# Performance work log

Measured on AMD Instinct MI355X. Metric: run time of the kernel, lower is better.

## Reference

```python
import jax, jax.numpy as jnp
import numpy as np

HEADS = 8

def setup_inputs() -> dict:
    key = jax.random.key(0)
    ks = jax.random.split(key, 5)
    B, C, H, W = 2, 256, 64, 64
    dim = C
    x = jax.random.normal(ks[0], (B, C, H, W), dtype=jnp.float32)
    # Linear weights stored as [in, out] so y = x @ W + b
    w_qkv = jax.random.normal(ks[1], (dim, 3 * dim), dtype=jnp.float32) * (dim ** -0.5)
    b_qkv = jax.random.normal(ks[2], (3 * dim,), dtype=jnp.float32) * 0.02
    w_out = jax.random.normal(ks[3], (dim, dim), dtype=jnp.float32) * (dim ** -0.5)
    b_out = jax.random.normal(ks[4], (dim,), dtype=jnp.float32) * 0.02
    return {"x": x, "w_qkv": w_qkv, "b_qkv": b_qkv, "w_out": w_out, "b_out": b_out}

def reference(x, w_qkv, b_qkv, w_out, b_out):
    B, C, H, W = x.shape
    h = HEADS
    d = C // h
    scale = d ** -0.5
    # [B, C, H, W] -> [B, N, C]
    tokens = x.reshape(B, C, H * W).transpose(0, 2, 1)
    qkv = tokens @ w_qkv + b_qkv  # [B, N, 3C]
    q, k, v = jnp.split(qkv, 3, axis=-1)
    def to_heads(t):
        Bn, N, _ = t.shape
        return t.reshape(Bn, N, h, d).transpose(0, 2, 1, 3)  # [B, h, N, d]
    q, k, v = map(to_heads, (q, k, v))
    dots = jnp.einsum('bhnd,bhmd->bhnm', q, k) * scale  # [B, h, N, N]
    attn = jax.nn.softmax(dots, axis=-1)
    out = jnp.einsum('bhnm,bhmd->bhnd', attn, v)  # [B, h, N, d]
    out = out.transpose(0, 2, 1, 3).reshape(B, H * W, C)  # [B, N, C]
    out = out @ w_out + b_out
    return out.transpose(0, 2, 1).reshape(B, C, H, W)
```

## Files before the change

### kernel.cpp

```cpp
#include <hip/hip_runtime.h>

typedef __attribute__((ext_vector_type(8))) short s16x8;
typedef __attribute__((ext_vector_type(4))) short s16x4;
typedef __attribute__((ext_vector_type(4))) float f32x4;
typedef __attribute__((ext_vector_type(2))) unsigned u32x2;

#define MFMA32(a, b, c) __builtin_amdgcn_mfma_f32_16x16x32_bf16((a), (b), (c), 0, 0, 0)

#if __has_builtin(__builtin_amdgcn_mfma_f32_16x16x16bf16_1k)
#define MFMA16K(a, b, c) __builtin_amdgcn_mfma_f32_16x16x16bf16_1k((a), (b), (c), 0, 0, 0)
#else
#define MFMA16K(a, b, c) (c)
#endif

#if __has_builtin(__builtin_amdgcn_exp2f)
#define EXP2F(x) __builtin_amdgcn_exp2f(x)
#else
#define EXP2F(x) __exp2f(x)
#endif

#if __has_builtin(__builtin_amdgcn_rcpf)
#define RCPF(x) __builtin_amdgcn_rcpf(x)
#else
#define RCPF(x) (1.0f / (x))
#endif

#define SL2E 0.25507313f

__device__ __forceinline__ unsigned pkrne(float a, float b) {
  unsigned ua = __builtin_bit_cast(unsigned, a);
  unsigned ub = __builtin_bit_cast(unsigned, b);
  ua += 0x7FFFu + ((ua >> 16) & 1u);
  ub += 0x7FFFu + ((ub >> 16) & 1u);
  return __builtin_amdgcn_perm(ub, ua, 0x07060302u);
}

__device__ __forceinline__ unsigned pktrunc(float a, float b) {
  return __builtin_amdgcn_perm(__builtin_bit_cast(unsigned, b),
                               __builtin_bit_cast(unsigned, a), 0x07060302u);
}

__device__ __forceinline__ unsigned short bfr(float f) {
  unsigned u = __builtin_bit_cast(unsigned, f);
  u += 0x7FFFu + ((u >> 16) & 1u);
  return (unsigned short)(u >> 16);
}

__device__ __forceinline__ float bflo(unsigned u) {
  return __builtin_bit_cast(float, u << 16);
}
__device__ __forceinline__ float bfhi(unsigned u) {
  return __builtin_bit_cast(float, u & 0xFFFF0000u);
}

__global__ __launch_bounds__(256) void prep_kernel(
    const float* __restrict__ x, const float* __restrict__ wqkv,
    const float* __restrict__ wout, ushort* __restrict__ xbf,
    ushort* __restrict__ wT, ushort* __restrict__ woT) {
  const int t = threadIdx.x;
  const int sub = t & 15, grp = t >> 4;
  const int id = blockIdx.x;
  const float* src;
  ushort* dst;
  int src_ld, k0, n0;
  float sc = 1.f;
  if (id < 512) {
    int mt = id & 63, kt = (id >> 6) & 3, b = id >> 8;
    src = x + (size_t)b * 256 * 4096;
    src_ld = 4096;
    dst = xbf + (size_t)b * 4096 * 256;
    k0 = kt * 64;
    n0 = mt * 64;
  } else if (id < 560) {
    int r = id - 512, nt = r % 12, kt = r / 12;
    src = wqkv;
    src_ld = 768;
    dst = wT;
    k0 = kt * 64;
    n0 = nt * 64;
    if (n0 < 256) sc = SL2E;
  } else {
    int r = id - 560, nt = r & 3, kt = r >> 2;
    src = wout;
    src_ld = 256;
    dst = woT;
    k0 = kt * 64;
    n0 = nt * 64;
  }
  const int k = k0 + grp * 4;
  const int n = n0 + sub * 4;
  unsigned d0[4], d1[4];
#pragma unroll
  for (int i = 0; i < 4; ++i) {
    float4 v = *(const float4*)(src + (size_t)(k + i) * src_ld + n);
    d0[i] = pkrne(v.x * sc, v.y * sc);
    d1[i] = pkrne(v.z * sc, v.w * sc);
  }
  u32x2 r0 = {__builtin_amdgcn_perm(d0[1], d0[0], 0x05040100u),
              __builtin_amdgcn_perm(d0[3], d0[2], 0x05040100u)};
  u32x2 r1 = {__builtin_amdgcn_perm(d0[1], d0[0], 0x07060302u),
              __builtin_amdgcn_perm(d0[3], d0[2], 0x07060302u)};
  u32x2 r2 = {__builtin_amdgcn_perm(d1[1], d1[0], 0x05040100u),
              __builtin_amdgcn_perm(d1[3], d1[2], 0x05040100u)};
  u32x2 r3 = {__builtin_amdgcn_perm(d1[1], d1[0], 0x07060302u),
              __builtin_amdgcn_perm(d1[3], d1[2], 0x07060302u)};
  *(u32x2*)(dst + (size_t)(n + 0) * 256 + k) = r0;
  *(u32x2*)(dst + (size_t)(n + 1) * 256 + k) = r1;
  *(u32x2*)(dst + (size_t)(n + 2) * 256 + k) = r2;
  *(u32x2*)(dst + (size_t)(n + 3) * 256 + k) = r3;
}

__global__ __launch_bounds__(256) void qkv_kernel(
    const ushort* __restrict__ xbf, const ushort* __restrict__ wT,
    const float* __restrict__ bq, ushort* __restrict__ QG,
    ushort* __restrict__ KG, ushort* __restrict__ VtG) {
  __shared__ __align__(16) ushort Wl[64][40];
  __shared__ __align__(16) ushort Xl[128][40];
  const int t0 = blockIdx.x * 128;
  const int n0 = blockIdx.y * 64;
  const int t = threadIdx.x;
  const int wid = t >> 6, lane = t & 63;
  const int wy = wid >> 1, wx = wid & 1;
  const int quad = lane >> 4, l16 = lane & 15;
  f32x4 acc[2][4] = {};
  const int wr = t >> 2, wsg = t & 3;
  for (int k0 = 0; k0 < 256; k0 += 32) {
    __syncthreads();
    *(uint4*)&Wl[wr][wsg * 8] =
        *(const uint4*)(wT + (size_t)(n0 + wr) * 256 + k0 + wsg * 8);
#pragma unroll
    for (int i = 0; i < 2; ++i) {
      int fid = t + 256 * i, row = fid >> 2, seg = fid & 3;
      *(uint4*)&Xl[row][seg * 8] =
          *(const uint4*)(xbf + (size_t)(t0 + row) * 256 + k0 + seg * 8);
    }
    __syncthreads();
    s16x8 wf[2], xf[4];
#pragma unroll
    for (int i = 0; i < 2; ++i)
      wf[i] = *(const s16x8*)&Wl[32 * wy + 16 * i + l16][quad * 8];
#pragma unroll
    for (int j = 0; j < 4; ++j)
      xf[j] = *(const s16x8*)&Xl[64 * wx + 16 * j + l16][quad * 8];
#pragma unroll
    for (int i = 0; i < 2; ++i)
#pragma unroll
      for (int j = 0; j < 4; ++j) acc[i][j] = MFMA32(wf[i], xf[j], acc[i][j]);
  }
  if (n0 < 512) {
    ushort* dst = (n0 < 256) ? QG : KG;
    const float bsc = (n0 < 256) ? SL2E : 1.f;
#pragma unroll
    for (int i = 0; i < 2; ++i) {
      int nb = n0 + 32 * wy + 16 * i + 4 * quad;
      float4 b4 = *(const float4*)(bq + nb);
      float bx0 = b4.x * bsc, bx1 = b4.y * bsc, bx2 = b4.z * bsc,
            bx3 = b4.w * bsc;
      int h = ((nb & 255) >> 5);
      int dd0 = nb & 31;
#pragma unroll
      for (int j = 0; j < 4; ++j) {
        int tok = t0 + 64 * wx + 16 * j + l16;
        int b = tok >> 12, tokn = tok & 4095;
        u32x2 pk = {pkrne(acc[i][j][0] + bx0, acc[i][j][1] + bx1),
                    pkrne(acc[i][j][2] + bx2, acc[i][j][3] + bx3)};
        *(u32x2*)(dst + ((size_t)(b * 8 + h) * 4096 + tokn) * 32 + dd0) = pk;
      }
    }
  } else {
#pragma unroll
    for (int i = 0; i < 2; ++i) {
      int nb = n0 + 32 * wy + 16 * i + 4 * quad;
      float4 b4 = *(const float4*)(bq + nb);
      float bb[4] = {b4.x, b4.y, b4.z, b4.w};
#pragma unroll
      for (int r = 0; r < 4; ++r) {
        int nn = nb + r - 512;
        int h = nn >> 5, ddv = nn & 31;
        ushort* vrow = VtG + (size_t)(h * 32 + ddv) * 4096;
#pragma unroll
        for (int j = 0; j < 4; ++j) {
          int tok = t0 + 64 * wx + 16 * j + l16;
          int b = tok >> 12, tokn = tok & 4095;
          vrow[(size_t)b * 8 * 32 * 4096 + tokn] = bfr(acc[i][j][r] + bb[r]);
        }
      }
    }
  }
}

__global__ __launch_bounds__(256, 6) void attn_split(
    const ushort* __restrict__ QG, const ushort* __restrict__ KG,
    const ushort* __restrict__ VtG, ushort* __restrict__ OF0,
    ushort* __restrict__ OFb, float* __restrict__ LF) {
  __shared__ __align__(16) ushort Kl[2][64][40];
  __shared__ __align__(16) ushort Vl[2][32][72];
  const int id = blockIdx.x;
  const int bh = (id & 7) * 2 + ((id >> 3) & 1);
  const int q0 = ((id >> 4) & 31) * 128;
  const int sp = id >> 9;
  const int kt0 = (sp * 64 + 2) / 3;
  const int niter = ((sp + 1) * 64 + 2) / 3 - kt0;
  const int t = threadIdx.x;
  const int wid = t >> 6, lane = t & 63;
  const int quad = lane >> 4, l16 = lane & 15;
  const size_t base = (size_t)bh * 4096 * 32;
  const ushort* qp = QG + base;
  const ushort* kp = KG + base;
  const ushort* vp = VtG + base;
  const int qw = q0 + 32 * wid;
  const s16x8 qf0 = *(const s16x8*)(qp + (size_t)(qw + l16) * 32 + quad * 8);
  const s16x8 qf1 = *(const s16x8*)(qp + (size_t)(qw + 16 + l16) * 32 + quad * 8);
  const int kr = t >> 2, ks = t & 3;
  const int vr = t >> 3, vsg = t & 7;
  *(uint4*)&Kl[0][kr][ks * 8] =
      *(const uint4*)(kp + (size_t)(kt0 * 64 + kr) * 32 + ks * 8);
  *(uint4*)&Vl[0][vr][vsg * 8] =
      *(const uint4*)(vp + (size_t)vr * 4096 + kt0 * 64 + vsg * 8);
  const ushort* kpre = kp + (size_t)((kt0 + 1) * 64 + kr) * 32 + ks * 8;
  const ushort* vpre = vp + (size_t)vr * 4096 + (kt0 + 1) * 64 + vsg * 8;
  __syncthreads();
  f32x4 o00 = {}, o01 = {}, o10 = {}, o11 = {}, ol0 = {}, ol1 = {};
  const f32x4 zero = {};
  const s16x4 ones = {(short)0x3F80, (short)0x3F80, (short)0x3F80,
                      (short)0x3F80};
  for (int i = 0; i < niter; ++i) {
    const int cur = i & 1;
    const bool more = (i + 1) < niter;
    uint4 kv, vv;
    if (more) {
      kv = *(const uint4*)kpre;
      vv = *(const uint4*)vpre;
      kpre += 2048;
      vpre += 64;
    }
    unsigned pl0[4], ph0[4], pl1[4], ph1[4];
#pragma unroll
    for (int nb = 0; nb < 4; ++nb) {
      s16x8 kf = *(const s16x8*)&Kl[cur][16 * nb + l16][quad * 8];
      f32x4 s0 = MFMA32(kf, qf0, zero);
      f32x4 s1 = MFMA32(kf, qf1, zero);
      pl0[nb] = pktrunc(EXP2F(s0[0]), EXP2F(s0[1]));
      ph0[nb] = pktrunc(EXP2F(s0[2]), EXP2F(s0[3]));
      pl1[nb] = pktrunc(EXP2F(s1[0]), EXP2F(s1[1]));
      ph1[nb] = pktrunc(EXP2F(s1[2]), EXP2F(s1[3]));
    }
#pragma unroll
    for (int nb = 0; nb < 4; ++nb) {
      u32x2 pu0 = {pl0[nb], ph0[nb]};
      u32x2 pu1 = {pl1[nb], ph1[nb]};
      s16x4 pv0 = __builtin_bit_cast(s16x4, pu0);
      s16x4 pv1 = __builtin_bit_cast(s16x4, pu1);
      s16x4 va = *(const s16x4*)&Vl[cur][l16][16 * nb + quad * 4];
      s16x4 vb = *(const s16x4*)&Vl[cur][16 + l16][16 * nb + quad * 4];
      o00 = MFMA16K(va, pv0, o00);
      o01 = MFMA16K(vb, pv0, o01);
      o10 = MFMA16K(va, pv1, o10);
      o11 = MFMA16K(vb, pv1, o11);
      ol0 = MFMA16K(ones, pv0, ol0);
      ol1 = MFMA16K(ones, pv1, ol1);
    }
    if (more) {
      *(uint4*)&Kl[cur ^ 1][kr][ks * 8] = kv;
      *(uint4*)&Vl[cur ^ 1][vr][vsg * 8] = vv;
    }
    __syncthreads();
  }
  ushort* OFs = (sp == 0) ? OF0 : OFb + (size_t)(sp - 1) * 2097152;
  float* LFs = LF + (size_t)sp * 65536;
  const int tok0 = qw + l16;
  const size_t ob0 = ((size_t)bh * 4096 + tok0) * 32;
  const size_t ob1 = ob0 + (size_t)16 * 32;
  u32x2 w00 = {pkrne(o00[0], o00[1]), pkrne(o00[2], o00[3])};
  u32x2 w01 = {pkrne(o01[0], o01[1]), pkrne(o01[2], o01[3])};
  u32x2 w10 = {pkrne(o10[0], o10[1]), pkrne(o10[2], o10[3])};
  u32x2 w11 = {pkrne(o11[0], o11[1]), pkrne(o11[2], o11[3])};
  *(u32x2*)(OFs + ob0 + 4 * quad) = w00;
  *(u32x2*)(OFs + ob0 + 16 + 4 * quad) = w01;
  *(u32x2*)(OFs + ob1 + 4 * quad) = w10;
  *(u32x2*)(OFs + ob1 + 16 + 4 * quad) = w11;
  if (quad == 0) {
    LFs[(size_t)bh * 4096 + tok0] = ol0[0];
    LFs[(size_t)bh * 4096 + tok0 + 16] = ol1[0];
  }
}

__global__ __launch_bounds__(256) void proj_split(
    const ushort* __restrict__ OF0, const ushort* __restrict__ OFb,
    const float* __restrict__ LF, const ushort* __restrict__ woT,
    const float* __restrict__ bo, float* __restrict__ out) {
  __shared__ __align__(16) ushort Wl[64][40];
  __shared__ __align__(16) ushort Xl[128][40];
  const int t0 = blockIdx.x * 128;
  const int c0 = blockIdx.y * 64;
  const int t = threadIdx.x;
  const int wid = t >> 6, lane = t & 63;
  const int wy = wid >> 1, wx = wid & 1;
  const int quad = lane >> 4, l16 = lane & 15;
  f32x4 acc[2][4] = {};
  const int wr = t >> 2, wsg = t & 3;
  const int c8 = (t & 7) * 4;
  for (int k0 = 0; k0 < 256; k0 += 32) {
    __syncthreads();
    *(uint4*)&Wl[wr][wsg * 8] =
        *(const uint4*)(woT + (size_t)(c0 + wr) * 256 + k0 + wsg * 8);
    const int hh = k0 >> 5;
#pragma unroll
    for (int p = 0; p < 4; ++p) {
      int row = 32 * p + (t >> 3);
      int tok = t0 + row, bb = tok >> 12, tokn = tok & 4095;
      size_t ro = (size_t)(bb * 8 + hh) * 4096 + tokn;
      size_t oi = ro * 32 + c8;
      uint2 a0 = *(const uint2*)(OF0 + oi);
      uint2 a1 = *(const uint2*)(OFb + oi);
      uint2 a2 = *(const uint2*)(OFb + 2097152 + oi);
      float l = LF[ro] + LF[65536 + ro] + LF[131072 + ro];
      float inv = RCPF(l);
      f32x4 s;
      s[0] = bflo(a0.x) + bflo(a1.x) + bflo(a2.x);
      s[1] = bfhi(a0.x) + bfhi(a1.x) + bfhi(a2.x);
      s[2] = bflo(a0.y) + bflo(a1.y) + bflo(a2.y);
      s[3] = bfhi(a0.y) + bfhi(a1.y) + bfhi(a2.y);
      s *= inv;
      u32x2 pk = {pkrne(s[0], s[1]), pkrne(s[2], s[3])};
      *(u32x2*)&Xl[row][c8] = pk;
    }
    __syncthreads();
    s16x8 wf[2], xf[4];
#pragma unroll
    for (int i = 0; i < 2; ++i)
      wf[i] = *(const s16x8*)&Wl[32 * wy + 16 * i + l16][quad * 8];
#pragma unroll
    for (int j = 0; j < 4; ++j)
      xf[j] = *(const s16x8*)&Xl[64 * wx + 16 * j + l16][quad * 8];
#pragma unroll
    for (int i = 0; i < 2; ++i)
#pragma unroll
      for (int j = 0; j < 4; ++j) acc[i][j] = MFMA32(wf[i], xf[j], acc[i][j]);
  }
#pragma unroll
  for (int i = 0; i < 2; ++i) {
    int cb = c0 + 32 * wy + 16 * i + 4 * quad;
    float4 b4 = *(const float4*)(bo + cb);
    float bb[4] = {b4.x, b4.y, b4.z, b4.w};
#pragma unroll
    for (int j = 0; j < 4; ++j) {
      int tok = t0 + 64 * wx + 16 * j + l16;
      int b = tok >> 12, tokn = tok & 4095;
#pragma unroll
      for (int r = 0; r < 4; ++r)
        out[((size_t)(b * 256 + cb + r)) * 4096 + tokn] = acc[i][j][r] + bb[r];
    }
  }
}

extern "C" void kernel_launch(void* const* d_in, const int* in_sizes, int n_in,
                              void* d_out, int out_size, void* d_ws, size_t ws_size,
                              hipStream_t stream) {
  (void)in_sizes; (void)n_in; (void)out_size; (void)ws_size;
  const float* x = (const float*)d_in[0];
  const float* wq = (const float*)d_in[1];
  const float* bq = (const float*)d_in[2];
  const float* wo = (const float*)d_in[3];
  const float* bo = (const float*)d_in[4];
  float* out = (float*)d_out;
  ushort* ws = (ushort*)d_ws;
  ushort* xbf = ws;
  ushort* OF0 = ws;
  ushort* QG  = ws + 2097152;
  ushort* KG  = ws + 4194304;
  ushort* VtG = ws + 6291456;
  ushort* wT  = ws + 8388608;
  ushort* woT = ws + 8585216;
  ushort* OFb = ws + 8650752;
  float* LF = (float*)(ws + 12845056);
  prep_kernel<<<576, 256, 0, stream>>>(x, wq, wo, xbf, wT, woT);
  qkv_kernel<<<dim3(64, 12), 256, 0, stream>>>(xbf, wT, bq, QG, KG, VtG);
  attn_split<<<1536, 256, 0, stream>>>(QG, KG, VtG, OF0, OFb, LF);
  proj_split<<<dim3(64, 4), 256, 0, stream>>>(OF0, OFb, LF, woT, bo, out);
}
```

Baseline: 140.0 us.

## Rework split attention around 32x32x16 MFMA with direct LDS staging

Rewrites the attention inner loop to use 32x32x16 bf16 MFMA for both the QK^T and PV products instead of 16x16 tiles. P is rearranged between the two products with permlane32 swaps rather than a round trip through memory. K/V tiles are staged straight from global memory into LDS with global_load_lds into a pre-swizzled layout. The row sum is now accumulated with VALU adds instead of an extra ones-vector MFMA. Occupancy bound drops from 6 to 4 blocks per CU, and output stores become scalar 2-byte writes, which may be less efficient.

```diff
diff --git a/kernel.cpp b/kernel.cpp
--- a/kernel.cpp
+++ b/kernel.cpp
@@ -1,16 +1,17 @@
 #include <hip/hip_runtime.h>
 
 typedef __attribute__((ext_vector_type(8))) short s16x8;
-typedef __attribute__((ext_vector_type(4))) short s16x4;
 typedef __attribute__((ext_vector_type(4))) float f32x4;
+typedef __attribute__((ext_vector_type(16))) float f32x16;
 typedef __attribute__((ext_vector_type(2))) unsigned u32x2;
+typedef __attribute__((ext_vector_type(4))) unsigned u32x4;
 
 #define MFMA32(a, b, c) __builtin_amdgcn_mfma_f32_16x16x32_bf16((a), (b), (c), 0, 0, 0)
 
-#if __has_builtin(__builtin_amdgcn_mfma_f32_16x16x16bf16_1k)
-#define MFMA16K(a, b, c) __builtin_amdgcn_mfma_f32_16x16x16bf16_1k((a), (b), (c), 0, 0, 0)
-#else
-#define MFMA16K(a, b, c) (c)
+#if __has_builtin(__builtin_amdgcn_mfma_f32_32x32x16_bf16)
+#define MFMA3216(a, b, c) __builtin_amdgcn_mfma_f32_32x32x16_bf16((a), (b), (c), 0, 0, 0)
+#else
+#define MFMA3216(a, b, c) (c)
 #endif
 
 #if __has_builtin(__builtin_amdgcn_exp2f)
@@ -51,6 +52,33 @@
 }
 __device__ __forceinline__ float bfhi(unsigned u) {
   return __builtin_bit_cast(float, u & 0xFFFF0000u);
+}
+
+__device__ __forceinline__ u32x2 plswap(unsigned a, unsigned b) {
+#if __has_builtin(__builtin_amdgcn_permlane32_swap)
+  return __builtin_amdgcn_permlane32_swap(a, b, false, false);
+#else
+  unsigned sa = (unsigned)__shfl_xor((int)a, 32, 64);
+  unsigned sb = (unsigned)__shfl_xor((int)b, 32, 64);
+  bool hi = (threadIdx.x & 63) >= 32;
+  u32x2 r;
+  r.x = hi ? sb : a;
+  r.y = hi ? b : sa;
+  return r;
+#endif
+}
+
+__device__ __forceinline__ void stage16(const ushort* g, ushort* l, int lane) {
+#if __has_builtin(__builtin_amdgcn_global_load_lds)
+  __builtin_amdgcn_global_load_lds(
+      (__attribute__((address_space(1))) unsigned int*)(unsigned long long)(
+          const void*)g,
+      (__attribute__((address_space(3))) unsigned int*)(unsigned)(
+          unsigned long long)(const void*)l,
+      16, 0, 0);
+#else
+  *(uint4*)(l + lane * 8) = *(const uint4*)g;
+#endif
 }
 
 __global__ __launch_bounds__(256) void prep_kernel(
@@ -189,12 +217,11 @@
   }
 }
 
-__global__ __launch_bounds__(256, 6) void attn_split(
+__global__ __launch_bounds__(256, 4) void attn_split(
     const ushort* __restrict__ QG, const ushort* __restrict__ KG,
     const ushort* __restrict__ VtG, ushort* __restrict__ OF0,
     ushort* __restrict__ OFb, float* __restrict__ LF) {
-  __shared__ __align__(16) ushort Kl[2][64][40];
-  __shared__ __align__(16) ushort Vl[2][32][72];
+  __shared__ __align__(64) ushort KVs[2][4096];
   const int id = blockIdx.x;
   const int bh = (id & 7) * 2 + ((id >> 3) & 1);
   const int q0 = ((id >> 4) & 31) * 128;
@@ -203,86 +230,73 @@
   const int niter = ((sp + 1) * 64 + 2) / 3 - kt0;
   const int t = threadIdx.x;
   const int wid = t >> 6, lane = t & 63;
-  const int quad = lane >> 4, l16 = lane & 15;
+  const int l5 = lane & 31, hi = lane >> 5;
   const size_t base = (size_t)bh * 4096 * 32;
   const ushort* qp = QG + base;
   const ushort* kp = KG + base;
   const ushort* vp = VtG + base;
   const int qw = q0 + 32 * wid;
-  const s16x8 qf0 = *(const s16x8*)(qp + (size_t)(qw + l16) * 32 + quad * 8);
-  const s16x8 qf1 = *(const s16x8*)(qp + (size_t)(qw + 16 + l16) * 32 + quad * 8);
-  const int kr = t >> 2, ks = t & 3;
-  const int vr = t >> 3, vsg = t & 7;
-  *(uint4*)&Kl[0][kr][ks * 8] =
-      *(const uint4*)(kp + (size_t)(kt0 * 64 + kr) * 32 + ks * 8);
-  *(uint4*)&Vl[0][vr][vsg * 8] =
-      *(const uint4*)(vp + (size_t)vr * 4096 + kt0 * 64 + vsg * 8);
-  const ushort* kpre = kp + (size_t)((kt0 + 1) * 64 + kr) * 32 + ks * 8;
-  const ushort* vpre = vp + (size_t)vr * 4096 + (kt0 + 1) * 64 + vsg * 8;
+  const ushort* qrow = qp + (size_t)(qw + l5) * 32 + hi * 8;
+  const s16x8 qf0 = *(const s16x8*)(qrow);
+  const s16x8 qf1 = *(const s16x8*)(qrow + 16);
+  const int sK = wid >> 1, hK = wid & 1;
+  const int kdst = sK * 1024 + hK * 512;
+  const ushort* kpre =
+      kp + (size_t)(kt0 * 64 + sK * 32 + l5) * 32 + hK * 16 + hi * 8;
+  const ushort* vpre =
+      vp + (size_t)l5 * 4096 + kt0 * 64 + sK * 32 + hK * 16 + hi * 8;
+  stage16(kpre, &KVs[0][kdst], lane);
+  stage16(vpre, &KVs[0][2048 + kdst], lane);
+  kpre += 2048;
+  vpre += 64;
   __syncthreads();
-  f32x4 o00 = {}, o01 = {}, o10 = {}, o11 = {}, ol0 = {}, ol1 = {};
-  const f32x4 zero = {};
-  const s16x4 ones = {(short)0x3F80, (short)0x3F80, (short)0x3F80,
-                      (short)0x3F80};
+  f32x16 o = {};
+  float lacc = 0.f;
   for (int i = 0; i < niter; ++i) {
     const int cur = i & 1;
-    const bool more = (i + 1) < niter;
-    uint4 kv, vv;
-    if (more) {
-      kv = *(const uint4*)kpre;
-      vv = *(const uint4*)vpre;
+    if (i + 1 < niter) {
+      stage16(kpre, &KVs[cur ^ 1][kdst], lane);
+      stage16(vpre, &KVs[cur ^ 1][2048 + kdst], lane);
       kpre += 2048;
       vpre += 64;
     }
-    unsigned pl0[4], ph0[4], pl1[4], ph1[4];
-#pragma unroll
-    for (int nb = 0; nb < 4; ++nb) {
-      s16x8 kf = *(const s16x8*)&Kl[cur][16 * nb + l16][quad * 8];
-      f32x4 s0 = MFMA32(kf, qf0, zero);
-      f32x4 s1 = MFMA32(kf, qf1, zero);
-      pl0[nb] = pktrunc(EXP2F(s0[0]), EXP2F(s0[1]));
-      ph0[nb] = pktrunc(EXP2F(s0[2]), EXP2F(s0[3]));
-      pl1[nb] = pktrunc(EXP2F(s1[0]), EXP2F(s1[1]));
-      ph1[nb] = pktrunc(EXP2F(s1[2]), EXP2F(s1[3]));
-    }
-#pragma unroll
-    for (int nb = 0; nb < 4; ++nb) {
-      u32x2 pu0 = {pl0[nb], ph0[nb]};
-      u32x2 pu1 = {pl1[nb], ph1[nb]};
-      s16x4 pv0 = __builtin_bit_cast(s16x4, pu0);
-      s16x4 pv1 = __builtin_bit_cast(s16x4, pu1);
-      s16x4 va = *(const s16x4*)&Vl[cur][l16][16 * nb + quad * 4];
-      s16x4 vb = *(const s16x4*)&Vl[cur][16 + l16][16 * nb + quad * 4];
-      o00 = MFMA16K(va, pv0, o00);
-      o01 = MFMA16K(vb, pv0, o01);
-      o10 = MFMA16K(va, pv1, o10);
-      o11 = MFMA16K(vb, pv1, o11);
-      ol0 = MFMA16K(ones, pv0, ol0);
-      ol1 = MFMA16K(ones, pv1, ol1);
-    }
-    if (more) {
-      *(uint4*)&Kl[cur ^ 1][kr][ks * 8] = kv;
-      *(uint4*)&Vl[cur ^ 1][vr][vsg * 8] = vv;
+    const ushort* kb = &KVs[cur][0];
+    const ushort* vb = &KVs[cur][2048];
+#pragma unroll
+    for (int s = 0; s < 2; ++s) {
+      const s16x8 ka0 = *(const s16x8*)(kb + s * 1024 + lane * 8);
+      const s16x8 ka1 = *(const s16x8*)(kb + s * 1024 + 512 + lane * 8);
+      f32x16 S = {};
+      S = MFMA3216(ka0, qf0, S);
+      S = MFMA3216(ka1, qf1, S);
+      unsigned w8[8];
+#pragma unroll
+      for (int ii = 0; ii < 8; ++ii)
+        w8[ii] = pktrunc(EXP2F(S[2 * ii]), EXP2F(S[2 * ii + 1]));
+#pragma unroll
+      for (int ii = 0; ii < 8; ++ii) lacc += bflo(w8[ii]) + bfhi(w8[ii]);
+      u32x2 sw0 = plswap(w8[0], w8[2]);
+      u32x2 sw1 = plswap(w8[1], w8[3]);
+      u32x2 sw2 = plswap(w8[4], w8[6]);
+      u32x2 sw3 = plswap(w8[5], w8[7]);
+      u32x4 pa0 = {sw0.x, sw1.x, sw0.y, sw1.y};
+      u32x4 pa1 = {sw2.x, sw3.x, sw2.y, sw3.y};
+      const s16x8 va0 = *(const s16x8*)(vb + s * 1024 + lane * 8);
+      const s16x8 va1 = *(const s16x8*)(vb + s * 1024 + 512 + lane * 8);
+      o = MFMA3216(__builtin_bit_cast(s16x8, pa0), va0, o);
+      o = MFMA3216(__builtin_bit_cast(s16x8, pa1), va1, o);
     }
     __syncthreads();
   }
   ushort* OFs = (sp == 0) ? OF0 : OFb + (size_t)(sp - 1) * 2097152;
   float* LFs = LF + (size_t)sp * 65536;
-  const int tok0 = qw + l16;
-  const size_t ob0 = ((size_t)bh * 4096 + tok0) * 32;
-  const size_t ob1 = ob0 + (size_t)16 * 32;
-  u32x2 w00 = {pkrne(o00[0], o00[1]), pkrne(o00[2], o00[3])};
-  u32x2 w01 = {pkrne(o01[0], o01[1]), pkrne(o01[2], o01[3])};
-  u32x2 w10 = {pkrne(o10[0], o10[1]), pkrne(o10[2], o10[3])};
-  u32x2 w11 = {pkrne(o11[0], o11[1]), pkrne(o11[2], o11[3])};
-  *(u32x2*)(OFs + ob0 + 4 * quad) = w00;
-  *(u32x2*)(OFs + ob0 + 16 + 4 * quad) = w01;
-  *(u32x2*)(OFs + ob1 + 4 * quad) = w10;
-  *(u32x2*)(OFs + ob1 + 16 + 4 * quad) = w11;
-  if (quad == 0) {
-    LFs[(size_t)bh * 4096 + tok0] = ol0[0];
-    LFs[(size_t)bh * 4096 + tok0 + 16] = ol1[0];
-  }
+#pragma unroll
+  for (int r = 0; r < 16; ++r) {
+    int q = qw + (r & 3) + 8 * (r >> 2) + 4 * hi;
+    OFs[((size_t)bh * 4096 + q) * 32 + l5] = bfr(o[r]);
+  }
+  float lw = lacc + __shfl_xor(lacc, 32, 64);
+  if (lane < 32) LFs[(size_t)bh * 4096 + qw + lane] = lw;
 }
 
 __global__ __launch_bounds__(256) void proj_split(
```

Measured after the change: 146.0 us. 1.04x slower.
